# Performance work log

Hardware: AMD Instinct MI355X
Metric: run time of the kernel (lower is better)

Reference implementation:

```python
import jax, jax.numpy as jnp
import numpy as np

B, T, C, V = 4, 2048, 512, 32000


def setup_inputs() -> dict:
    key = jax.random.key(0)
    ks = jax.random.split(key, 8)
    return {
        "idx": jax.random.randint(ks[0], (B, T), 0, V, dtype=jnp.int64 if jax.config.jax_enable_x64 else jnp.int32),
        "targets": jax.random.randint(ks[1], (B, T), 0, V, dtype=jnp.int64 if jax.config.jax_enable_x64 else jnp.int32),
        "token_emb": jax.random.normal(ks[2], (V, C), jnp.float32) * 0.02,
        "pos_emb": jax.random.normal(ks[3], (T, C), jnp.float32) * 0.02,
        "Wk": jax.random.normal(ks[4], (C, C), jnp.float32) / np.sqrt(C),
        "Wq": jax.random.normal(ks[5], (C, C), jnp.float32) / np.sqrt(C),
        "Wv": jax.random.normal(ks[6], (C, C), jnp.float32) / np.sqrt(C),
        "Wo": jax.random.normal(ks[7], (C, V), jnp.float32) / np.sqrt(C),
        "bo": jnp.zeros((V,), jnp.float32),
    }


def reference(idx, targets, token_emb, pos_emb, Wk, Wq, Wv, Wo, bo):
    # embeddings: token lookup + positional add  -> [B, T, C]
    x = token_emb[idx] + pos_emb[None, :idx.shape[1]]
    # single self-attention head (scale uses input dim C, per source)
    q = x @ Wq  # [B, T, C]
    k = x @ Wk
    v = x @ Wv
    wei = jnp.einsum("btc,bsc->bts", q, k) * (C ** -0.5)  # [B, T, T]
    mask = jnp.tril(jnp.ones((idx.shape[1], idx.shape[1]), bool))
    wei = jnp.where(mask[None], wei, -jnp.inf)
    wei = jax.nn.softmax(wei, axis=-1)
    attn = jnp.einsum("bts,bsc->btc", wei, v)  # [B, T, C]
    logits = attn @ Wo + bo  # [B, T, V]
    # cross-entropy (mean over B*T), matching F.cross_entropy
    logp = jax.nn.log_softmax(logits, axis=-1)
    nll = -jnp.take_along_axis(logp, targets[..., None], axis=-1)[..., 0]
    loss = nll.mean()
    return logits, loss
```

## Files before the change

kernel.cpp:

```cpp
#include <hip/hip_runtime.h>
#include <cstdint>

typedef unsigned short u16;
typedef __attribute__((ext_vector_type(8))) short short8;
typedef __attribute__((ext_vector_type(4))) float f32x4;

constexpr int kB = 4, kT = 2048, kC = 512, kV = 32000;
constexpr int kBT = kB * kT;
constexpr float kScale = 0.044194173824159216f;

__device__ __forceinline__ u16 f2b(float f) {
  union { float f; unsigned u; } v; v.f = f;
  unsigned r = v.u + 0x7fffu + ((v.u >> 16) & 1u);
  return (u16)(r >> 16);
}

__device__ __forceinline__ void g2lds16(const u16* g, u16* l) {
  __builtin_amdgcn_global_load_lds(
      (const __attribute__((address_space(1))) void*)g,
      (__attribute__((address_space(3))) void*)l, 16, 0, 0);
}

__global__ __launch_bounds__(256) void transpose_cast(const float* __restrict__ in,
                                                      u16* __restrict__ out,
                                                      int R, int Ncol) {
  __shared__ u16 tile[32][33];
  int c0 = blockIdx.x * 32, r0 = blockIdx.y * 32;
  int tx = threadIdx.x, ty = threadIdx.y;
#pragma unroll
  for (int j = 0; j < 32; j += 8)
    tile[ty + j][tx] = f2b(in[(long)(r0 + ty + j) * Ncol + (c0 + tx)]);
  __syncthreads();
#pragma unroll
  for (int j = 0; j < 32; j += 8)
    out[(long)(c0 + ty + j) * R + (r0 + tx)] = tile[tx][ty + j];
}

__global__ __launch_bounds__(128) void embed_kernel(const int* __restrict__ idx,
                                                    const float* __restrict__ te,
                                                    const float* __restrict__ pe,
                                                    u16* __restrict__ xb) {
  int row = blockIdx.x;
  int t = row & (kT - 1);
  int tok = idx[row];
  int c = threadIdx.x * 4;
  float4 a = *(const float4*)(te + (long)tok * kC + c);
  float4 p = *(const float4*)(pe + (long)t * kC + c);
  ushort4 o;
  o.x = f2b(a.x + p.x); o.y = f2b(a.y + p.y);
  o.z = f2b(a.z + p.z); o.w = f2b(a.w + p.w);
  *(ushort4*)(xb + (long)row * kC + c) = o;
}

template <int OUT_MODE, bool CAUSAL, bool KCAP>
__global__ __launch_bounds__(256) void gemm_bt(
    const u16* __restrict__ A, const u16* __restrict__ Bt, void* __restrict__ OutP,
    const float* __restrict__ bias,
    int M, int N, int K, int lda, int ldb, int ldo,
    long batchA, long batchB, long batchO, float alpha) {
  int bz = blockIdx.z;
  A += bz * batchA;
  Bt += bz * batchB;
  int m0 = blockIdx.y * 128, n0 = blockIdx.x * 128;
  if (CAUSAL && n0 > m0 + 127) return;

  __shared__ u16 As[2][128 * 32];
  __shared__ u16 Bs[2][128 * 32];
  int tid = threadIdx.x;
  int lane = tid & 63, w = tid >> 6;
  int wr = w >> 1, wc = w & 1;
  int lm = lane & 15, lk = lane >> 4;

  f32x4 acc[4][4] = {};

  const u16* aptr = A + (long)(m0 + (w << 4) + (lane >> 2)) * lda + ((lane & 3) << 3);
  const u16* bptr = Bt + (long)(n0 + (w << 4) + (lane >> 2)) * ldb + ((lane & 3) << 3);

#define STAGE(buf)                                                   \
  {                                                                  \
    g2lds16(aptr,                  &As[buf][(w << 4) * 32]);         \
    g2lds16(aptr + (long)64 * lda, &As[buf][(64 + (w << 4)) * 32]);  \
    g2lds16(bptr,                  &Bs[buf][(w << 4) * 32]);         \
    g2lds16(bptr + (long)64 * ldb, &Bs[buf][(64 + (w << 4)) * 32]);  \
  }

  int nk = K >> 5;
  if (KCAP) { int cap = (m0 >> 5) + 4; nk = (cap < nk) ? cap : nk; }
  STAGE(0);
  __syncthreads();

  for (int kt = 0; kt < nk; ++kt) {
    int cur = kt & 1;
    aptr += 32; bptr += 32;
    if (kt + 1 < nk) STAGE(cur ^ 1);
    short8 af[4], bf[4];
#pragma unroll
    for (int i = 0; i < 4; ++i) {
      af[i] = *(const short8*)&As[cur][(wr * 64 + i * 16 + lm) * 32 + lk * 8];
      bf[i] = *(const short8*)&Bs[cur][(wc * 64 + i * 16 + lm) * 32 + lk * 8];
    }
#pragma unroll
    for (int mi = 0; mi < 4; ++mi)
#pragma unroll
      for (int ni = 0; ni < 4; ++ni)
        acc[mi][ni] = __builtin_amdgcn_mfma_f32_16x16x32_bf16(af[mi], bf[ni], acc[mi][ni], 0, 0, 0);
    __syncthreads();
  }
#undef STAGE

#pragma unroll
  for (int mi = 0; mi < 4; ++mi) {
#pragma unroll
    for (int ni = 0; ni < 4; ++ni) {
      int row = m0 + wr * 64 + mi * 16 + lk * 4;
      int col = n0 + wc * 64 + ni * 16 + lm;
      if (OUT_MODE == 0) {
        float* Out = (float*)OutP + bz * batchO;
        float bv = bias ? bias[col] : 0.0f;
#pragma unroll
        for (int r = 0; r < 4; ++r)
          Out[(long)(row + r) * ldo + col] = acc[mi][ni][r] * alpha + bv;
      } else if (OUT_MODE == 1) {
        u16* Out = (u16*)OutP + bz * batchO;
#pragma unroll
        for (int r = 0; r < 4; ++r)
          Out[(long)(row + r) * ldo + col] = f2b(acc[mi][ni][r] * alpha);
      } else {
        u16* Out = (u16*)OutP + bz * batchO;
        ushort4 pk;
        pk.x = f2b(acc[mi][ni][0] * alpha);
        pk.y = f2b(acc[mi][ni][1] * alpha);
        pk.z = f2b(acc[mi][ni][2] * alpha);
        pk.w = f2b(acc[mi][ni][3] * alpha);
        *(ushort4*)&Out[(long)col * ldo + row] = pk;
      }
    }
  }
}

__global__ __launch_bounds__(512, 2) void gemm256_logits_ce(
    const u16* __restrict__ A, const u16* __restrict__ Bt,
    float* __restrict__ Out, const float* __restrict__ bias,
    float* __restrict__ cepart) {
  constexpr int lda = kC, ldb = kC, ldo = kV;
  constexpr int nk = kC / 64;
  constexpr int NB = kV / 256;

  __shared__ u16 lds[65536];

  int wg = blockIdx.x;
  int xcd = wg & 7;
  int i = wg >> 3;
  int g = i >> 5, r = i & 31;
  int bx = (g < 15) ? (g * 8 + (r >> 2)) : (120 + (r >> 2));
  int by = xcd * 4 + (r & 3);
  int m0 = by * 256, n0 = bx * 256;

  int tid = threadIdx.x;
  int lane = tid & 63, w = tid >> 6;
  int wm = w >> 2, wn = w & 3;
  int lm = lane & 15, lk = lane >> 4;
  int lk16 = lk * 16, sw = (lm & 7) << 4;
  int brow0 = (wn & 1) * 64;

  int srow = tid >> 3;
  int scol = ((tid & 7) ^ ((tid >> 3) & 7)) * 8;
  const u16* Arow = A + (long)(m0 + srow) * lda + scol;
  const u16* Brow = Bt + (long)(n0 + srow) * ldb + scol;

  f32x4 acc[8][4] = {};
  short8 aF[4][2], bF[4][2];

  auto stage = [&](int s) {
    if (s >= 4 * nk) return;
    int tile = s >> 2, hf = s & 3, buf = tile & 1;
    int kofs = tile * 64;
    if (hf >= 2) {
      u16* base = &lds[(buf * 2 + (hf - 2)) * 8192 + w * 512];
      const u16* gp = Arow + (long)((hf - 2) * 128) * lda + kofs;
      g2lds16(gp, base);
      g2lds16(gp + (long)64 * lda, base + 4096);
    } else {
      u16* base = &lds[32768 + (buf * 2 + hf) * 8192 + w * 512];
      const u16* gp = Brow + (long)(hf * 128) * ldb + kofs;
      g2lds16(gp, base);
      g2lds16(gp + (long)64 * ldb, base + 4096);
    }
  };

#pragma unroll
  for (int s = 0; s < 6; ++s) stage(s);
  asm volatile("s_waitcnt vmcnt(4)" ::: "memory");
  __builtin_amdgcn_sched_barrier(0);
  __builtin_amdgcn_s_barrier();

#pragma unroll 2
  for (int t = 0; t < nk; ++t) {
    int cur = t & 1;
    const char* Ab = (const char*)&lds[(cur * 2 + wm) * 8192];
    const char* Bb = (const char*)&lds[32768 + (cur * 2 + (wn >> 1)) * 8192];

#define RDA(i, ks) (*(const short8*)(Ab + (((qr)*4 + (i)) * 16 + lm) * 128 + (((ks)*64 + lk16) ^ sw)))
#define RDB(j, ks) (*(const short8*)(Bb + (brow0 + ((qc)*2 + (j)) * 16 + lm) * 128 + (((ks)*64 + lk16) ^ sw)))
#define MFMA_QUAD                                                              \
  _Pragma("unroll") for (int i = 0; i < 4; ++i)                                \
  _Pragma("unroll") for (int j = 0; j < 2; ++j)                                \
  _Pragma("unroll") for (int ks = 0; ks < 2; ++ks)                             \
      acc[qr * 4 + i][qc * 2 + j] = __builtin_amdgcn_mfma_f32_16x16x32_bf16(   \
          aF[i][ks], bF[qc * 2 + j][ks], acc[qr * 4 + i][qc * 2 + j], 0, 0, 0);

    {
      constexpr int qr = 0, qc = 0;
#pragma unroll
      for (int i = 0; i < 4; ++i) { aF[i][0] = RDA(i, 0); aF[i][1] = RDA(i, 1); }
#pragma unroll
      for (int j = 0; j < 2; ++j) { bF[j][0] = RDB(j, 0); bF[j][1] = RDB(j, 1); }
      stage(4 * (t + 1) + 2);
      stage(4 * (t + 1) + 3);
      __builtin_amdgcn_s_barrier();
      asm volatile("s_waitcnt lgkmcnt(0)" ::: "memory");
      __builtin_amdgcn_s_setprio(1);
      MFMA_QUAD
      __builtin_amdgcn_s_setprio(0);
      __builtin_amdgcn_s_barrier();
    }
    {
      constexpr int qr = 0, qc = 1;
#pragma unroll
      for (int j = 0; j < 2; ++j) { bF[2 + j][0] = RDB(j, 0); bF[2 + j][1] = RDB(j, 1); }
      __builtin_amdgcn_s_barrier();
      asm volatile("s_waitcnt lgkmcnt(0)" ::: "memory");
      __builtin_amdgcn_s_setprio(1);
      MFMA_QUAD
      __builtin_amdgcn_s_setprio(0);
      __builtin_amdgcn_s_barrier();
    }
    {
      constexpr int qr = 1, qc = 0;
#pragma unroll
      for (int i = 0; i < 4; ++i) { aF[i][0] = RDA(i, 0); aF[i][1] = RDA(i, 1); }
      __builtin_amdgcn_s_barrier();
      asm volatile("s_waitcnt lgkmcnt(0)" ::: "memory");
      __builtin_amdgcn_s_setprio(1);
      MFMA_QUAD
      __builtin_amdgcn_s_setprio(0);
      __builtin_amdgcn_s_barrier();
    }
    {
      constexpr int qr = 1, qc = 1;
      stage(4 * (t + 2) + 0);
      stage(4 * (t + 2) + 1);
      __builtin_amdgcn_s_barrier();
      asm volatile("s_waitcnt lgkmcnt(0)" ::: "memory");
      __builtin_amdgcn_s_setprio(1);
      MFMA_QUAD
      __builtin_amdgcn_s_setprio(0);
      if (t < nk - 2) {
        asm volatile("s_waitcnt vmcnt(4)" ::: "memory");
        __builtin_amdgcn_sched_barrier(0);
      } else if (t == nk - 2) {
        asm volatile("s_waitcnt vmcnt(0)" ::: "memory");
        __builtin_amdgcn_sched_barrier(0);
      }
      __builtin_amdgcn_s_barrier();
    }
#undef RDA
#undef RDB
#undef MFMA_QUAD
  }

  float* lds_ce = (float*)lds;
#pragma unroll
  for (int rf = 0; rf < 8; ++rf) {
    int grow = m0 + wm * 128 + rf * 16 + lk * 4;
    float rowsum[4] = {};
#pragma unroll
    for (int cf = 0; cf < 4; ++cf) {
      int col = n0 + wn * 64 + cf * 16 + lm;
      float bv = bias[col];
#pragma unroll
      for (int r = 0; r < 4; ++r) {
        float v = acc[rf][cf][r] + bv;
        __builtin_nontemporal_store(v, &Out[(long)(grow + r) * ldo + col]);
        rowsum[r] += __expf(v);
      }
    }
#pragma unroll
    for (int off = 1; off < 16; off <<= 1)
#pragma unroll
      for (int r = 0; r < 4; ++r)
        rowsum[r] += __shfl_xor(rowsum[r], off, 64);
    if (lm == 0) {
#pragma unroll
      for (int r = 0; r < 4; ++r)
        lds_ce[w * 128 + rf * 16 + lk * 4 + r] = rowsum[r];
    }
  }
  __syncthreads();
  if (tid < 256) {
    int wmg = tid >> 7, r128 = tid & 127;
    float s = lds_ce[(wmg * 4 + 0) * 128 + r128] + lds_ce[(wmg * 4 + 1) * 128 + r128]
            + lds_ce[(wmg * 4 + 2) * 128 + r128] + lds_ce[(wmg * 4 + 3) * 128 + r128];
    cepart[(long)(m0 + tid) * NB + bx] = s;
  }
}

__global__ __launch_bounds__(256) void softmax_causal(const float* __restrict__ S,
                                                      u16* __restrict__ P) {
  int row = blockIdx.x;
  int t = row & (kT - 1);
  int lim = ((t >> 7) + 1) << 7;
  const float* srow = S + (long)row * kT;
  u16* prow = P + (long)row * kT;
  __shared__ float buf[kT];
  __shared__ float red[256];
  int tid = threadIdx.x;
  float mx = -1e30f;
  for (int s = tid; s < lim; s += 256) {
    float v = (s <= t) ? srow[s] : -1e30f;
    buf[s] = v;
    mx = fmaxf(mx, v);
  }
  red[tid] = mx; __syncthreads();
  for (int o = 128; o > 0; o >>= 1) {
    if (tid < o) red[tid] = fmaxf(red[tid], red[tid + o]);
    __syncthreads();
  }
  mx = red[0]; __syncthreads();
  float sm = 0.0f;
  for (int s = tid; s < lim; s += 256) {
    float e = (s <= t) ? __expf(buf[s] - mx) : 0.0f;
    buf[s] = e;
    sm += e;
  }
  red[tid] = sm; __syncthreads();
  for (int o = 128; o > 0; o >>= 1) {
    if (tid < o) red[tid] += red[tid + o];
    __syncthreads();
  }
  float inv = 1.0f / red[0];
  for (int s = tid; s < lim; s += 256) prow[s] = f2b(buf[s] * inv);
}

__global__ __launch_bounds__(256) void ce_reduce(const float* __restrict__ logits,
                                                 const float* __restrict__ part,
                                                 const int* __restrict__ targets,
                                                 float* __restrict__ nll, int P) {
  int row = blockIdx.x * 4 + (threadIdx.x >> 6);
  int lane = threadIdx.x & 63;
  const float* pr = part + (long)row * P;
  float s = 0.0f;
  for (int p = lane; p < P; p += 64) s += pr[p];
#pragma unroll
  for (int off = 1; off < 64; off <<= 1) s += __shfl_xor(s, off, 64);
  if (lane == 0)
    nll[row] = __logf(s) - logits[(long)row * kV + targets[row]];
}

__global__ __launch_bounds__(256) void loss_reduce(const float* __restrict__ nll,
                                                   float* __restrict__ out) {
  __shared__ float red[256];
  int tid = threadIdx.x;
  float s = 0.0f;
  for (int i = tid; i < kBT; i += 256) s += nll[i];
  red[tid] = s; __syncthreads();
  for (int o = 128; o > 0; o >>= 1) {
    if (tid < o) red[tid] += red[tid + o];
    __syncthreads();
  }
  if (tid == 0) out[0] = red[0] / (float)kBT;
}

extern "C" void kernel_launch(void* const* d_in, const int* in_sizes, int n_in,
                              void* d_out, int out_size, void* d_ws, size_t ws_size,
                              hipStream_t stream) {
  const int* idx       = (const int*)d_in[0];
  const int* targets   = (const int*)d_in[1];
  const float* token_e = (const float*)d_in[2];
  const float* pos_e   = (const float*)d_in[3];
  const float* Wk      = (const float*)d_in[4];
  const float* Wq      = (const float*)d_in[5];
  const float* Wv      = (const float*)d_in[6];
  const float* Wo      = (const float*)d_in[7];
  const float* bo      = (const float*)d_in[8];
  float* out = (float*)d_out;

  char* ws = (char*)d_ws;
  size_t need = 0;
  auto alloc = [&](size_t bytes) { char* p = ws + need; need += (bytes + 255) & ~(size_t)255; return p; };
  u16* xb   = (u16*)alloc((size_t)kBT * kC * 2);
  u16* wqt  = (u16*)alloc((size_t)kC * kC * 2);
  u16* wkt  = (u16*)alloc((size_t)kC * kC * 2);
  u16* wvt  = (u16*)alloc((size_t)kC * kC * 2);
  u16* wot  = (u16*)alloc((size_t)kV * kC * 2);
  u16* qb   = (u16*)alloc((size_t)kBT * kC * 2);
  u16* kb   = (u16*)alloc((size_t)kBT * kC * 2);
  u16* vt   = (u16*)alloc((size_t)kC * kBT * 2);
  u16* attn = (u16*)alloc((size_t)kBT * kC * 2);
  float* nll = (float*)alloc((size_t)kBT * 4);
  if (ws_size < need) return;

  float* cepart = (float*)qb;

  float* Sbuf = out;
  u16* Pbuf   = (u16*)((char*)d_out + (100ull << 20));

  dim3 tb(32, 8);
  transpose_cast<<<dim3(kC / 32, kC / 32), tb, 0, stream>>>(Wq, wqt, kC, kC);
  transpose_cast<<<dim3(kC / 32, kC / 32), tb, 0, stream>>>(Wk, wkt, kC, kC);
  transpose_cast<<<dim3(kC / 32, kC / 32), tb, 0, stream>>>(Wv, wvt, kC, kC);
  transpose_cast<<<dim3(kV / 32, kC / 32), tb, 0, stream>>>(Wo, wot, kC, kV);

  embed_kernel<<<kBT, 128, 0, stream>>>(idx, token_e, pos_e, xb);

  gemm_bt<1, false, false><<<dim3(4, 64, 2), 256, 0, stream>>>(xb, wqt, qb, nullptr,
      kBT, kC, kC, kC, kC, kC, 0, (long)kC * kC, (long)kBT * kC, 1.0f);
  gemm_bt<2, false, false><<<dim3(4, 64, 1), 256, 0, stream>>>(xb, wvt, vt, nullptr,
      kBT, kC, kC, kC, kC, kBT, 0, 0, 0, 1.0f);

  gemm_bt<0, true, false><<<dim3(16, 16, 4), 256, 0, stream>>>(qb, kb, Sbuf, nullptr,
      kT, kT, kC, kC, kC, kT, (long)kT * kC, (long)kT * kC, (long)kT * kT, kScale);

  softmax_causal<<<kBT, 256, 0, stream>>>(Sbuf, Pbuf);

  gemm_bt<1, false, true><<<dim3(4, 16, 4), 256, 0, stream>>>(Pbuf, vt, attn, nullptr,
      kT, kC, kT, kT, kBT, kC, (long)kT * kT, (long)kT, (long)kT * kC, 1.0f);

  gemm256_logits_ce<<<dim3((kV / 256) * (kBT / 256)), 512, 0, stream>>>(
      attn, wot, out, bo, cepart);

  ce_reduce<<<kBT / 4, 256, 0, stream>>>(out, cepart, targets, nll, kV / 256);
  loss_reduce<<<1, 256, 0, stream>>>(nll, out + (long)kBT * kV);
}
```

Measured before the change: 563.5 us.

## Merge QKV weight transposes, restage logits GEMM loads, defer logits stores

The three square weight transpose-casts become one launch with a z-dimension selector, which removes two kernel launches. In the 256x256 logits+CE GEMM, each tile's A and B halves are now issued as single 4-load stages at two points per iteration instead of four 2-load stages, with a new LDS buffer layout. The epilogue hoists the bias loads, computes the exp row sums and CE partials first, then writes the logits with nontemporal stores afterwards, so the reduction is not interleaved with global stores. The restaged loads alter the vmcnt-based prefetch timing, and the waitcnt thresholds are left unchanged.

```diff
diff --git a/kernel.cpp b/kernel.cpp
--- a/kernel.cpp
+++ b/kernel.cpp
@@ -34,6 +34,24 @@
 #pragma unroll
   for (int j = 0; j < 32; j += 8)
     out[(long)(c0 + ty + j) * R + (r0 + tx)] = tile[tx][ty + j];
+}
+
+__global__ __launch_bounds__(256) void transpose_cast3(
+    const float* __restrict__ w0, const float* __restrict__ w1,
+    const float* __restrict__ w2, u16* __restrict__ o0,
+    u16* __restrict__ o1, u16* __restrict__ o2) {
+  const float* in = blockIdx.z == 0 ? w0 : (blockIdx.z == 1 ? w1 : w2);
+  u16* out = blockIdx.z == 0 ? o0 : (blockIdx.z == 1 ? o1 : o2);
+  __shared__ u16 tile[32][33];
+  int c0 = blockIdx.x * 32, r0 = blockIdx.y * 32;
+  int tx = threadIdx.x, ty = threadIdx.y;
+#pragma unroll
+  for (int j = 0; j < 32; j += 8)
+    tile[ty + j][tx] = f2b(in[(long)(r0 + ty + j) * kC + (c0 + tx)]);
+  __syncthreads();
+#pragma unroll
+  for (int j = 0; j < 32; j += 8)
+    out[(long)(c0 + ty + j) * kC + (r0 + tx)] = tile[tx][ty + j];
 }
 
 __global__ __launch_bounds__(128) void embed_kernel(const int* __restrict__ idx,
@@ -171,25 +189,28 @@
   f32x4 acc[8][4] = {};
   short8 aF[4][2], bF[4][2];
 
-  auto stage = [&](int s) {
-    if (s >= 4 * nk) return;
-    int tile = s >> 2, hf = s & 3, buf = tile & 1;
-    int kofs = tile * 64;
-    if (hf >= 2) {
-      u16* base = &lds[(buf * 2 + (hf - 2)) * 8192 + w * 512];
-      const u16* gp = Arow + (long)((hf - 2) * 128) * lda + kofs;
-      g2lds16(gp, base);
-      g2lds16(gp + (long)64 * lda, base + 4096);
-    } else {
-      u16* base = &lds[32768 + (buf * 2 + hf) * 8192 + w * 512];
-      const u16* gp = Brow + (long)(hf * 128) * ldb + kofs;
-      g2lds16(gp, base);
-      g2lds16(gp + (long)64 * ldb, base + 4096);
-    }
+  u16* ldsAw = &lds[w * 512];
+  u16* ldsBw = &lds[32768 + w * 512];
+  auto stageA = [&](int tile) {
+    if (tile >= nk) return;
+    u16* base = ldsAw + (tile & 1) * 16384;
+    const u16* gp = Arow + tile * 64;
+    g2lds16(gp, base);
+    g2lds16(gp + (long)64 * lda, base + 4096);
+    g2lds16(gp + (long)128 * lda, base + 8192);
+    g2lds16(gp + (long)192 * lda, base + 12288);
   };
-
-#pragma unroll
-  for (int s = 0; s < 6; ++s) stage(s);
+  auto stageB = [&](int tile) {
+    if (tile >= nk) return;
+    u16* base = ldsBw + (tile & 1) * 16384;
+    const u16* gp = Brow + tile * 64;
+    g2lds16(gp, base);
+    g2lds16(gp + (long)64 * ldb, base + 4096);
+    g2lds16(gp + (long)128 * ldb, base + 8192);
+    g2lds16(gp + (long)192 * ldb, base + 12288);
+  };
+
+  stageB(0); stageA(0); stageB(1);
   asm volatile("s_waitcnt vmcnt(4)" ::: "memory");
   __builtin_amdgcn_sched_barrier(0);
   __builtin_amdgcn_s_barrier();
@@ -197,8 +218,8 @@
 #pragma unroll 2
   for (int t = 0; t < nk; ++t) {
     int cur = t & 1;
-    const char* Ab = (const char*)&lds[(cur * 2 + wm) * 8192];
-    const char* Bb = (const char*)&lds[32768 + (cur * 2 + (wn >> 1)) * 8192];
+    const char* Ab = (const char*)&lds[cur * 16384 + wm * 8192];
+    const char* Bb = (const char*)&lds[32768 + cur * 16384 + (wn >> 1) * 8192];
 
 #define RDA(i, ks) (*(const short8*)(Ab + (((qr)*4 + (i)) * 16 + lm) * 128 + (((ks)*64 + lk16) ^ sw)))
 #define RDB(j, ks) (*(const short8*)(Bb + (brow0 + ((qc)*2 + (j)) * 16 + lm) * 128 + (((ks)*64 + lk16) ^ sw)))
@@ -215,8 +236,7 @@
       for (int i = 0; i < 4; ++i) { aF[i][0] = RDA(i, 0); aF[i][1] = RDA(i, 1); }
 #pragma unroll
       for (int j = 0; j < 2; ++j) { bF[j][0] = RDB(j, 0); bF[j][1] = RDB(j, 1); }
-      stage(4 * (t + 1) + 2);
-      stage(4 * (t + 1) + 3);
+      stageA(t + 1);
       __builtin_amdgcn_s_barrier();
       asm volatile("s_waitcnt lgkmcnt(0)" ::: "memory");
       __builtin_amdgcn_s_setprio(1);
@@ -248,8 +268,7 @@
     }
     {
       constexpr int qr = 1, qc = 1;
-      stage(4 * (t + 2) + 0);
-      stage(4 * (t + 2) + 1);
+      stageB(t + 2);
       __builtin_amdgcn_s_barrier();
       asm volatile("s_waitcnt lgkmcnt(0)" ::: "memory");
       __builtin_amdgcn_s_setprio(1);
@@ -270,21 +289,17 @@
   }
 
   float* lds_ce = (float*)lds;
+  float bv[4];
+#pragma unroll
+  for (int cf = 0; cf < 4; ++cf) bv[cf] = bias[n0 + wn * 64 + cf * 16 + lm];
 #pragma unroll
   for (int rf = 0; rf < 8; ++rf) {
-    int grow = m0 + wm * 128 + rf * 16 + lk * 4;
     float rowsum[4] = {};
 #pragma unroll
-    for (int cf = 0; cf < 4; ++cf) {
-      int col = n0 + wn * 64 + cf * 16 + lm;
-      float bv = bias[col];
-#pragma unroll
-      for (int r = 0; r < 4; ++r) {
-        float v = acc[rf][cf][r] + bv;
-        __builtin_nontemporal_store(v, &Out[(long)(grow + r) * ldo + col]);
-        rowsum[r] += __expf(v);
-      }
-    }
+    for (int cf = 0; cf < 4; ++cf)
+#pragma unroll
+      for (int r = 0; r < 4; ++r)
+        rowsum[r] += __expf(acc[rf][cf][r] + bv[cf]);
 #pragma unroll
     for (int off = 1; off < 16; off <<= 1)
 #pragma unroll
@@ -302,6 +317,17 @@
     float s = lds_ce[(wmg * 4 + 0) * 128 + r128] + lds_ce[(wmg * 4 + 1) * 128 + r128]
             + lds_ce[(wmg * 4 + 2) * 128 + r128] + lds_ce[(wmg * 4 + 3) * 128 + r128];
     cepart[(long)(m0 + tid) * NB + bx] = s;
+  }
+#pragma unroll
+  for (int rf = 0; rf < 8; ++rf) {
+    int grow = m0 + wm * 128 + rf * 16 + lk * 4;
+#pragma unroll
+    for (int cf = 0; cf < 4; ++cf) {
+      int col = n0 + wn * 64 + cf * 16 + lm;
+#pragma unroll
+      for (int r = 0; r < 4; ++r)
+        __builtin_nontemporal_store(acc[rf][cf][r] + bv[cf], &Out[(long)(grow + r) * ldo + col]);
+    }
   }
 }
 
@@ -406,9 +432,7 @@
   u16* Pbuf   = (u16*)((char*)d_out + (100ull << 20));
 
   dim3 tb(32, 8);
-  transpose_cast<<<dim3(kC / 32, kC / 32), tb, 0, stream>>>(Wq, wqt, kC, kC);
-  transpose_cast<<<dim3(kC / 32, kC / 32), tb, 0, stream>>>(Wk, wkt, kC, kC);
-  transpose_cast<<<dim3(kC / 32, kC / 32), tb, 0, stream>>>(Wv, wvt, kC, kC);
+  transpose_cast3<<<dim3(16, 16, 3), tb, 0, stream>>>(Wq, Wk, Wv, wqt, wkt, wvt);
   transpose_cast<<<dim3(kV / 32, kC / 32), tb, 0, stream>>>(Wo, wot, kC, kV);
 
   embed_kernel<<<kBT, 128, 0, stream>>>(idx, token_e, pos_e, xb);
```

After: 569.9 us. No clear change (+1.1%).
